# Optimization experiments

Hardware: AMD Instinct MI355X
Metric: run time of the kernel (lower is better)

The kernel has to match this reference:

```python
import jax, jax.numpy as jnp
import numpy as np
import math

SQRT2 = math.sqrt(2.0)


def _rotation_grids(theta_deg, grid_size):
    # torch affine_grid (align_corners=True) base coords for output [G, G]:
    # grid[h, w] = (xs[w], ys[h]) transformed by R = [[c, s, 0], [-s, c, 0]]
    xs = jnp.linspace(-1.0, 1.0, grid_size, dtype=jnp.float32)
    X, Y = jnp.meshgrid(xs, xs)            # [G,G], X varies along width
    th = jnp.deg2rad(theta_deg.astype(jnp.float32))[:, None, None]  # [T,1,1]
    c, s = jnp.cos(th), jnp.sin(th)
    gx = c * X + s * Y                      # [T,G,G]
    gy = -s * X + c * Y
    return gx, gy


def _bilinear_sample(x, gx, gy):
    # x: [N,C,H,W]; gx,gy: [T,G,G] normalized coords in [-1,1]
    # bilinear, zeros padding, align_corners=True -> returns [N,C,T,G,G]
    N, C, H, W = x.shape
    ix = (gx + 1.0) * 0.5 * (W - 1)
    iy = (gy + 1.0) * 0.5 * (H - 1)
    ix0 = jnp.floor(ix)
    iy0 = jnp.floor(iy)
    wx1 = ix - ix0
    wy1 = iy - iy0
    wx0 = 1.0 - wx1
    wy0 = 1.0 - wy1

    def gather(iyf, ixf):
        valid = (ixf >= 0) & (ixf <= W - 1) & (iyf >= 0) & (iyf <= H - 1)
        ii = jnp.clip(ixf, 0, W - 1).astype(jnp.int32)
        jj = jnp.clip(iyf, 0, H - 1).astype(jnp.int32)
        v = x[:, :, jj, ii]                 # [N,C,T,G,G]
        return v * valid.astype(x.dtype)

    return (gather(iy0, ix0) * (wy0 * wx0)
            + gather(iy0, ix0 + 1) * (wy0 * wx1)
            + gather(iy0 + 1, ix0) * (wy1 * wx0)
            + gather(iy0 + 1, ix0 + 1) * (wy1 * wx1))


def radon_forward(x, theta_deg):
    N, C, W, H = x.shape
    # circle=False: pad image to the diagonal size so rotations keep all content
    diagonal = SQRT2 * W
    pad = int(math.ceil(diagonal - W))
    new_center = (W + pad) // 2
    old_center = W // 2
    pad_before = new_center - old_center
    x = jnp.pad(x, ((0, 0), (0, 0), (pad_before, pad - pad_before),
                    (pad_before, pad - pad_before)))
    G = x.shape[-1]                         # padded grid size == ceil(sqrt2*W)
    gx, gy = _rotation_grids(theta_deg, G)  # [T,G,G]
    rotated = _bilinear_sample(x, gx, gy)   # [N,C,T,G,G]
    sino = rotated.sum(axis=3)              # integrate over rows -> [N,C,T,G]
    return jnp.swapaxes(sino, 2, 3)         # [N,C,G,T]


def setup_inputs() -> dict:
    key = jax.random.key(0)
    x = jax.random.normal(key, (2, 1, 256, 256), dtype=jnp.float32)
    theta = jnp.arange(180, dtype=jnp.int64) if jax.config.jax_enable_x64 else jnp.arange(180, dtype=jnp.int32)
    return {"x": x, "theta": theta}


def reference(x, theta):
    return radon_forward(x, theta)
```

## Files before the change

kernel.cpp:

```cpp
#include <hip/hip_runtime.h>
#include <hip/hip_fp16.h>
#include <math.h>


#define G       363
#define NT      180
#define STEP    (2.0f / 362.0f)
#define DEG2RAD 0.017453292519943295f

#define NJB     12
#define NJBF    6
#define CW      264
#define CH      264

__global__ __launch_bounds__(256) void radon_fwd(
    const float* __restrict__ x, const int* __restrict__ theta,
    float* __restrict__ out)
{
    const int t = blockIdx.x / NJBF, jb = blockIdx.x % NJBF;
    const int jl = threadIdx.x, chunk = threadIdx.y;
    const int j = jb * 64 + jl;
    const float th = (float)theta[t] * DEG2RAD;
    const float c = cosf(th), s = sinf(th);
    const float xj = fmaf((float)j, STEP, -1.0f);
    const float s181 = s * 181.0f, c181 = c * 181.0f;
    const float bx = fmaf(c, xj, 1.0f) * 181.0f;
    const float by = fmaf(-s, xj, 1.0f) * 181.0f;
    const float* img0 = x;
    const float* img1 = x + 65536;
    float acc0 = 0.f, acc1 = 0.f;
    for (int i = chunk; i < G; i += 4) {
        const float xi = fmaf((float)i, STEP, -1.0f);
        const float ix = fmaf(s181, xi, bx);
        const float iy = fmaf(c181, xi, by);
        const float fx = floorf(ix), fy = floorf(iy);
        const int ix0 = (int)fx, iy0 = (int)fy;
        const float wx1 = ix - fx, wy1 = iy - fy;
        const float wx0 = 1.f - wx1, wy0 = 1.f - wy1;
        const int cc0 = ix0 - 53, cc1 = cc0 + 1, rr0 = iy0 - 53, rr1 = rr0 + 1;
        const float wxa = ((unsigned)cc0 < 256u) ? wx0 : 0.f;
        const float wxb = ((unsigned)cc1 < 256u) ? wx1 : 0.f;
        const float wya = ((unsigned)rr0 < 256u) ? wy0 : 0.f;
        const float wyb = ((unsigned)rr1 < 256u) ? wy1 : 0.f;
        const int c0c = min(max(cc0, 0), 255), c1c = min(max(cc1, 0), 255);
        const int r0b = min(max(rr0, 0), 255) << 8, r1b = min(max(rr1, 0), 255) << 8;
        const float w00 = wya * wxa, w01 = wya * wxb, w10 = wyb * wxa, w11 = wyb * wxb;
        acc0 = fmaf(img0[r0b + c0c], w00, acc0);
        acc0 = fmaf(img0[r0b + c1c], w01, acc0);
        acc0 = fmaf(img0[r1b + c0c], w10, acc0);
        acc0 = fmaf(img0[r1b + c1c], w11, acc0);
        acc1 = fmaf(img1[r0b + c0c], w00, acc1);
        acc1 = fmaf(img1[r0b + c1c], w01, acc1);
        acc1 = fmaf(img1[r1b + c0c], w10, acc1);
        acc1 = fmaf(img1[r1b + c1c], w11, acc1);
    }
    __shared__ float red[2][4][64];
    red[0][chunk][jl] = acc0;
    red[1][chunk][jl] = acc1;
    __syncthreads();
    if (threadIdx.y < 2 && j < G) {
        const int n = threadIdx.y;
        out[n * (G * NT) + j * NT + t] =
            red[n][0][jl] + red[n][1][jl] + red[n][2][jl] + red[n][3][jl];
    }
}

__global__ __launch_bounds__(256) void prep_k(
    const float* __restrict__ x,
    unsigned* __restrict__ xIh, unsigned* __restrict__ xTIh)
{
    const int bid = blockIdx.x;
    const int tx = threadIdx.x, ty = threadIdx.y;

    __shared__ unsigned tl[32][33];
    const int cx0 = (bid % 9) * 32, cy0 = (bid / 9) * 32;
    #pragma unroll
    for (int dy = 0; dy < 32; dy += 8) {
        const int cy = cy0 + ty + dy, cx = cx0 + tx;
        const int pr = cy - 4, pc = cx - 4;
        unsigned v = 0u;
        if ((unsigned)pr < 256u && (unsigned)pc < 256u) {
            const int p = pr * 256 + pc;
            const unsigned short a = __half_as_ushort(__float2half_rn(x[p]));
            const unsigned short b = __half_as_ushort(__float2half_rn(x[p + 65536]));
            v = (unsigned)a | ((unsigned)b << 16);
        }
        if (cy < CH && cx < CW) xIh[cy * CW + cx] = v;
        tl[ty + dy][tx] = v;
    }
    __syncthreads();
    #pragma unroll
    for (int dy = 0; dy < 32; dy += 8) {
        const int rp = cx0 + ty + dy, cp = cy0 + tx;
        if (rp < CH && cp < CW) xTIh[rp * CW + cp] = tl[tx][ty + dy];
    }
}

__device__ __forceinline__ __half2 tap(const unsigned* __restrict__ cv,
    float fi, float dU, float dV, float U00, float V00)
{
    const float U = fmaf(dU, fi, U00);
    const float V = fmaf(dV, fi, V00);
    const float fU = floorf(U), fV = floorf(V);
    const float wU1 = U - fU, wV1 = V - fV;
    const float fUc = fminf(fmaxf(fU, 0.0f), 262.0f);
    const float fVc = fminf(fmaxf(fV, 0.0f), 262.0f);
    const int rel = (int)fmaf(fUc, (float)CW, fVc);
    const __half2* p = (const __half2*)(cv + rel);
    const __half2 x00 = p[0];
    const __half2 x01 = p[1];
    const __half2 x10 = p[CW];
    const __half2 x11 = p[CW + 1];
    const __half2 wv2 = __float2half2_rn(wV1);
    const __half2 wu2 = __float2half2_rn(wU1);
    const __half2 t0 = __hfma2(wv2, __hsub2(x01, x00), x00);
    const __half2 t1 = __hfma2(wv2, __hsub2(x11, x10), x10);
    return __hfma2(wu2, __hsub2(t1, t0), t0);
}

__global__ __launch_bounds__(256) void radon_l2(
    const unsigned* __restrict__ xIh, const unsigned* __restrict__ xTIh,
    const int* __restrict__ theta, float* __restrict__ out)
{
    const int blk  = blockIdx.x;
    const int t    = blk / NJB;
    const int jb   = blk - t * NJB;
    const int tid  = threadIdx.x;
    const int lane = tid & 63;
    const int wid  = tid >> 6;
    const int jl   = lane & 31;
    const int kc   = lane >> 5;
    const int chunk = wid * 2 + kc;

    const float th = (float)theta[t] * DEG2RAD;
    const float c = cosf(th), s = sinf(th);
    const float s181 = s * 181.0f, c181 = c * 181.0f;

    const int   j  = jb * 32 + jl;
    const float xj = fmaf((float)j, STEP, -1.0f);
    const float bx = fmaf(c,  xj, 1.0f) * 181.0f;
    const float by = fmaf(-s, xj, 1.0f) * 181.0f;

    const int caseA = (fabsf(c) >= fabsf(s));
    const unsigned* __restrict__ cv = caseA ? xIh : xTIh;

    const float slopeU = caseA ? c181 : s181;
    const float slopeV = caseA ? s181 : c181;
    const float dU = slopeU * STEP;
    const float dV = slopeV * STEP;
    const float U00 = (caseA ? by : bx) - slopeU - 49.0f;
    const float V00 = (caseA ? bx : by) - slopeV - 49.0f;

    float a0 = 0.f, a1 = 0.f;

    float fig = (float)chunk;
    for (int g = 0; g < 7; ++g) {
        __half2 acc = __float2half2_rn(0.0f);
        #pragma unroll
        for (int k = 0; k < 6; ++k) {
            acc = __hadd2(acc, tap(cv, fig + (float)(k * 8), dU, dV, U00, V00));
        }
        a0 += __low2float(acc);
        a1 += __high2float(acc);
        fig += 48.0f;
    }
    {
        __half2 acc = __float2half2_rn(0.0f);
        #pragma unroll
        for (int k = 42; k < 46; ++k) {
            const int i = chunk + k * 8;
            if (i < G)
                acc = __hadd2(acc, tap(cv, (float)i, dU, dV, U00, V00));
        }
        a0 += __low2float(acc);
        a1 += __high2float(acc);
    }

    a0 += __shfl_xor(a0, 32);
    a1 += __shfl_xor(a1, 32);

    __shared__ float red[2][4][32];
    if (lane < 32) {
        red[0][wid][jl] = a0;
        red[1][wid][jl] = a1;
    }
    __syncthreads();

    if (tid < 64) {
        const int n = tid >> 5, jj = tid & 31;
        const float v = red[n][0][jj] + red[n][1][jj]
                      + red[n][2][jj] + red[n][3][jj];
        const int jo = jb * 32 + jj;
        if (jo < G)
            out[(n * G + jo) * NT + t] = v;
    }
}

extern "C" void kernel_launch(void* const* d_in, const int* in_sizes, int n_in,
                              void* d_out, int out_size, void* d_ws, size_t ws_size,
                              hipStream_t stream) {
    const float* x     = (const float*)d_in[0];
    const int*   theta = (const int*)d_in[1];
    float*       out   = (float*)d_out;

    const size_t XIH_OFF  = 0;
    const size_t XTIH_OFF = (size_t)CH * CW * 4;
    const size_t NEED     = 2 * XTIH_OFF;

    if (ws_size < NEED) {
        hipLaunchKernelGGL(radon_fwd, dim3(NT * NJBF), dim3(64, 4), 0, stream,
                           x, theta, out);
        return;
    }

    unsigned* xIh  = (unsigned*)((char*)d_ws + XIH_OFF);
    unsigned* xTIh = (unsigned*)((char*)d_ws + XTIH_OFF);

    hipLaunchKernelGGL(prep_k, dim3(81), dim3(32, 8), 0, stream,
                       x, xIh, xTIh);
    hipLaunchKernelGGL(radon_l2, dim3(NT * NJB), dim3(256), 0, stream,
                       xIh, xTIh, theta, out);
}
```

Baseline: 39.10 us.

## Stage per-wave 32x32 image tiles into LDS via global_load_lds before gathering

Replaces the direct global-memory bilinear gathers with a per-wave scheme. Each wave handles 16 projection columns by 24 rows per step, computes the bounding box of its sample footprint, and copies a 32x32 packed-half tile into LDS with async global_load_lds. The four bilinear taps are then read from LDS. This aims to turn scattered L2 gathers into coalesced 16-byte loads plus cheap LDS reads, but every step waits serially on vmcnt with no double buffering. The tile must also be large enough to cover the rotated footprint.

Measured after the change: 33.19 us. -15.1%, faster.

```diff
diff --git a/kernel.cpp b/kernel.cpp
--- a/kernel.cpp
+++ b/kernel.cpp
@@ -5,13 +5,19 @@
 
 #define G       363
 #define NT      180
+#define PADB    53
 #define STEP    (2.0f / 362.0f)
 #define DEG2RAD 0.017453292519943295f
 
+#define TSW     32
 #define NJB     12
 #define NJBF    6
 #define CW      264
 #define CH      264
+
+#define GLOAD16(gp, lp) __builtin_amdgcn_global_load_lds(                     \
+    (const __attribute__((address_space(1))) void*)(gp),                      \
+    (__attribute__((address_space(3))) void*)(lp), 16, 0, 0)
 
 __global__ __launch_bounds__(256) void radon_fwd(
     const float* __restrict__ x, const int* __restrict__ theta,
@@ -96,100 +102,161 @@
     }
 }
 
-__device__ __forceinline__ __half2 tap(const unsigned* __restrict__ cv,
-    float fi, float dU, float dV, float U00, float V00)
-{
-    const float U = fmaf(dU, fi, U00);
-    const float V = fmaf(dV, fi, V00);
-    const float fU = floorf(U), fV = floorf(V);
-    const float wU1 = U - fU, wV1 = V - fV;
-    const float fUc = fminf(fmaxf(fU, 0.0f), 262.0f);
-    const float fVc = fminf(fmaxf(fV, 0.0f), 262.0f);
-    const int rel = (int)fmaf(fUc, (float)CW, fVc);
-    const __half2* p = (const __half2*)(cv + rel);
-    const __half2 x00 = p[0];
-    const __half2 x01 = p[1];
-    const __half2 x10 = p[CW];
-    const __half2 x11 = p[CW + 1];
-    const __half2 wv2 = __float2half2_rn(wV1);
-    const __half2 wu2 = __float2half2_rn(wU1);
-    const __half2 t0 = __hfma2(wv2, __hsub2(x01, x00), x00);
-    const __half2 t1 = __hfma2(wv2, __hsub2(x11, x10), x10);
-    return __hfma2(wu2, __hsub2(t1, t0), t0);
-}
-
-__global__ __launch_bounds__(256) void radon_l2(
+template<bool SAFE>
+__device__ __forceinline__ void stage32(char* tileW_b,
+    const unsigned* __restrict__ srcC, int r0p, int c0p, int lane)
+{
+    const int ty0 = lane >> 3;
+    const int tx  = (lane & 7) << 2;
+    #pragma unroll
+    for (int u = 0; u < 4; ++u) {
+        const int ty = ty0 + (u << 3);
+        int idx;
+        if (SAFE) {
+            idx = (r0p + 4 + ty) * CW + (c0p + 4 + tx);
+        } else {
+            const int rc = min(max(r0p + ty, -4), 256) + 4;
+            const int cc = min(max(c0p + tx, -4), 256) + 4;
+            idx = rc * CW + cc;
+        }
+        GLOAD16(srcC + idx, tileW_b + (u << 10));
+    }
+}
+
+template<bool TAIL>
+__device__ __forceinline__ void gather6(const unsigned* __restrict__ tl,
+    float Uf0, float Vf0, float dU, float dV, int iexc,
+    float& a0, float& a1)
+{
+    __half2 acc = __float2half2_rn(0.0f);
+    #pragma unroll
+    for (int k = 0; k < 6; ++k) {
+        const float Uf = fmaf((float)k, dU, Uf0);
+        const float Vf = fmaf((float)k, dV, Vf0);
+        const float fU = floorf(Uf), fV = floorf(Vf);
+        const float wU1 = Uf - fU;
+        const float wV1 = Vf - fV;
+        const int rel = (int)fmaf(fU, (float)TSW, fV);
+        const __half2 x00 = *(const __half2*)(tl + rel);
+        const __half2 x01 = *(const __half2*)(tl + rel + 1);
+        const __half2 x10 = *(const __half2*)(tl + rel + TSW);
+        const __half2 x11 = *(const __half2*)(tl + rel + TSW + 1);
+        const __half2 wv2 = __float2half2_rn(wV1);
+        const __half2 wu2 = __float2half2_rn(wU1);
+        const __half2 t0 = __hfma2(wv2, __hsub2(x01, x00), x00);
+        const __half2 t1 = __hfma2(wv2, __hsub2(x11, x10), x10);
+        __half2 v = __hfma2(wu2, __hsub2(t1, t0), t0);
+        if (TAIL && k >= iexc) v = __float2half2_rn(0.0f);
+        acc = __hadd2(acc, v);
+    }
+    a0 += __low2float(acc);
+    a1 += __high2float(acc);
+}
+
+__global__ __launch_bounds__(256) void radon_wv(
     const unsigned* __restrict__ xIh, const unsigned* __restrict__ xTIh,
     const int* __restrict__ theta, float* __restrict__ out)
 {
+    __shared__ unsigned tile[4 * TSW * TSW];
+    __shared__ float red[4][2][16];
+
     const int blk  = blockIdx.x;
     const int t    = blk / NJB;
     const int jb   = blk - t * NJB;
     const int tid  = threadIdx.x;
     const int lane = tid & 63;
     const int wid  = tid >> 6;
-    const int jl   = lane & 31;
-    const int kc   = lane >> 5;
-    const int chunk = wid * 2 + kc;
+    const int wj   = wid & 1;
+    const int wi   = wid >> 1;
+    const int jl   = lane & 15;
+    const int kk   = lane >> 4;
+
+    unsigned* tileW = tile + wid * (TSW * TSW);
+    char*     tileW_b = (char*)tileW;
 
     const float th = (float)theta[t] * DEG2RAD;
     const float c = cosf(th), s = sinf(th);
     const float s181 = s * 181.0f, c181 = c * 181.0f;
 
-    const int   j  = jb * 32 + jl;
-    const float xj = fmaf((float)j, STEP, -1.0f);
-    const float bx = fmaf(c,  xj, 1.0f) * 181.0f;
-    const float by = fmaf(-s, xj, 1.0f) * 181.0f;
-
     const int caseA = (fabsf(c) >= fabsf(s));
-    const unsigned* __restrict__ cv = caseA ? xIh : xTIh;
+    const unsigned* __restrict__ srcC = caseA ? xIh : xTIh;
 
     const float slopeU = caseA ? c181 : s181;
     const float slopeV = caseA ? s181 : c181;
     const float dU = slopeU * STEP;
     const float dV = slopeV * STEP;
-    const float U00 = (caseA ? by : bx) - slopeU - 49.0f;
-    const float V00 = (caseA ? bx : by) - slopeV - 49.0f;
+
+    const int   j  = jb * 32 + wj * 16 + jl;
+    const float xj = fmaf((float)j, STEP, -1.0f);
+    const float bx = fmaf(c,  xj, 1.0f) * 181.0f;
+    const float by = fmaf(-s, xj, 1.0f) * 181.0f;
+    const float U00L = (caseA ? by : bx) - slopeU;
+    const float V00L = (caseA ? bx : by) - slopeV;
+
+    const int   j0  = jb * 32 + wj * 16;
+    const float xjm = fmaf((float)j0,        STEP, -1.0f);
+    const float xjM = fmaf((float)(j0 + 15), STEP, -1.0f);
+    const float bxm = fmaf(c,  xjm, 1.0f) * 181.0f;
+    const float bym = fmaf(-s, xjm, 1.0f) * 181.0f;
+    const float bxM = fmaf(c,  xjM, 1.0f) * 181.0f;
+    const float byM = fmaf(-s, xjM, 1.0f) * 181.0f;
+    const float U00m = (caseA ? bym : bxm) - slopeU;
+    const float U00M = (caseA ? byM : bxM) - slopeU;
+    const float V00m = (caseA ? bxm : bym) - slopeV;
+    const float V00M = (caseA ? bxM : byM) - slopeV;
+
+    const float fiofs = (float)(kk * 6);
 
     float a0 = 0.f, a1 = 0.f;
 
-    float fig = (float)chunk;
-    for (int g = 0; g < 7; ++g) {
-        __half2 acc = __float2half2_rn(0.0f);
-        #pragma unroll
-        for (int k = 0; k < 6; ++k) {
-            acc = __hadd2(acc, tap(cv, fig + (float)(k * 8), dU, dV, U00, V00));
+    for (int sub = 0; sub < 8; ++sub) {
+        const int i0 = (wi * 8 + sub) * 24;
+        const float fi0 = (float)i0, fi1 = (float)(i0 + 23);
+
+        const float Umin = fminf(fminf(fmaf(dU, fi0, U00m), fmaf(dU, fi0, U00M)),
+                                 fminf(fmaf(dU, fi1, U00m), fmaf(dU, fi1, U00M)));
+        const float Vmin = fminf(fminf(fmaf(dV, fi0, V00m), fmaf(dV, fi0, V00M)),
+                                 fminf(fmaf(dV, fi1, V00m), fmaf(dV, fi1, V00M)));
+        const int r0 = __builtin_amdgcn_readfirstlane((int)floorf(Umin) - 1);
+        const int c0 = __builtin_amdgcn_readfirstlane((int)floorf(Vmin) - 1);
+        const int r0p = r0 - PADB, c0p = c0 - PADB;
+
+        asm volatile("s_waitcnt lgkmcnt(0)" ::: "memory");
+        __builtin_amdgcn_sched_barrier(0);
+
+        if (r0p >= -4 && r0p <= 228 && c0p >= -4 && c0p <= 228)
+            stage32<true >(tileW_b, srcC, r0p, c0p, lane);
+        else
+            stage32<false>(tileW_b, srcC, r0p, c0p, lane);
+
+        asm volatile("s_waitcnt vmcnt(0)" ::: "memory");
+        __builtin_amdgcn_sched_barrier(0);
+
+        const float fi  = fi0 + fiofs;
+        const float Uf0 = fmaf(dU, fi, U00L) - (float)r0;
+        const float Vf0 = fmaf(dV, fi, V00L) - (float)c0;
+        const int ibase = i0 + kk * 6;
+
+        if (i0 + 23 < G) {
+            gather6<false>(tileW, Uf0, Vf0, dU, dV, 6, a0, a1);
+        } else {
+            gather6<true>(tileW, Uf0, Vf0, dU, dV, G - ibase, a0, a1);
         }
-        a0 += __low2float(acc);
-        a1 += __high2float(acc);
-        fig += 48.0f;
-    }
-    {
-        __half2 acc = __float2half2_rn(0.0f);
-        #pragma unroll
-        for (int k = 42; k < 46; ++k) {
-            const int i = chunk + k * 8;
-            if (i < G)
-                acc = __hadd2(acc, tap(cv, (float)i, dU, dV, U00, V00));
-        }
-        a0 += __low2float(acc);
-        a1 += __high2float(acc);
-    }
-
-    a0 += __shfl_xor(a0, 32);
-    a1 += __shfl_xor(a1, 32);
-
-    __shared__ float red[2][4][32];
-    if (lane < 32) {
-        red[0][wid][jl] = a0;
-        red[1][wid][jl] = a1;
+    }
+
+    a0 += __shfl_xor(a0, 16); a1 += __shfl_xor(a1, 16);
+    a0 += __shfl_xor(a0, 32); a1 += __shfl_xor(a1, 32);
+
+    if (lane < 16) {
+        red[wid][0][lane] = a0;
+        red[wid][1][lane] = a1;
     }
     __syncthreads();
 
     if (tid < 64) {
         const int n = tid >> 5, jj = tid & 31;
-        const float v = red[n][0][jj] + red[n][1][jj]
-                      + red[n][2][jj] + red[n][3][jj];
+        const int wj2 = jj >> 4, jl2 = jj & 15;
+        const float v = red[wj2][n][jl2] + red[wj2 + 2][n][jl2];
         const int jo = jb * 32 + jj;
         if (jo < G)
             out[(n * G + jo) * NT + t] = v;
@@ -218,6 +285,6 @@
 
     hipLaunchKernelGGL(prep_k, dim3(81), dim3(32, 8), 0, stream,
                        x, xIh, xTIh);
-    hipLaunchKernelGGL(radon_l2, dim3(NT * NJB), dim3(256), 0, stream,
+    hipLaunchKernelGGL(radon_wv, dim3(NT * NJB), dim3(256), 0, stream,
                        xIh, xTIh, theta, out);
 }
```
